# Kernel tuning notes

Hardware: AMD Instinct MI355X
Metric: run time of the kernel (lower is better)

Reference implementation:

```python
import jax, jax.numpy as jnp
import numpy as np

B, D = 4096, 1024
TEMPERATURE = 0.07


def setup_inputs() -> dict:
    key = jax.random.key(0)
    k1, k2, k3, k4, k5, k6 = jax.random.split(key, 6)
    return {
        "mri_features": jax.random.normal(k1, (B, D), dtype=jnp.float32),
        "pet_features": jax.random.normal(k2, (B, D), dtype=jnp.float32),
        "labels": jax.random.randint(k3, (B,), 0, 3, dtype=jnp.int64),
        "subtype_mri": jax.random.randint(k4, (B,), 0, 4, dtype=jnp.int64),
        "subtype_pet": jax.random.randint(k5, (B,), 0, 4, dtype=jnp.int64),
        "clinical_similarity": jax.random.uniform(k6, (B, B), dtype=jnp.float32),
    }


def _build_weights(labels, subtype_mri, subtype_pet, clinical_similarity):
    # vectorized form of the O(B^2) python loop
    same_label = labels[:, None] == labels[None, :]
    label_zero = labels[:, None] == 0
    sub_match = (subtype_mri[:, None] == subtype_mri[None, :]) & (
        subtype_pet[:, None] == subtype_pet[None, :]
    )
    n = labels.shape[0]
    not_diag = ~jnp.eye(n, dtype=bool)
    mask = same_label & (label_zero | sub_match) & not_diag
    weights = jnp.where(mask, clinical_similarity, 0.0)
    row_sums = weights.sum(axis=1, keepdims=True)
    row_sums = jnp.where(row_sums == 0, 1.0, row_sums)
    return weights / row_sums


def _contrastive(fi, fj, weights):
    fi = fi / jnp.linalg.norm(fi, axis=1, keepdims=True)
    fj = fj / jnp.linalg.norm(fj, axis=1, keepdims=True)
    sim = jnp.matmul(fi, fj.T) / TEMPERATURE  # [B, B]
    log_sm = jax.nn.log_softmax(sim, axis=1)
    return -jnp.sum(weights * log_sm) / fi.shape[0]


def reference(mri_features, pet_features, labels, subtype_mri, subtype_pet, clinical_similarity):
    weights = _build_weights(labels, subtype_mri, subtype_pet, clinical_similarity)
    pairs = [
        (mri_features, pet_features),
        (pet_features, mri_features),
        (mri_features, mri_features),
        (pet_features, pet_features),
    ]
    total = 0.0
    for fi, fj in pairs:
        total = total + _contrastive(fi, fj, weights)
    return total / len(pairs)
```

## Files before the change

### kernel.cpp

```cpp
#include <hip/hip_runtime.h>
#include <hip/hip_bf16.h>
#include <math.h>

typedef __attribute__((ext_vector_type(8))) short bf16x8;
typedef __attribute__((ext_vector_type(4))) short bf16x4;
typedef __attribute__((ext_vector_type(4))) float f32x4;

#define NB 4096
#define ND 1024
#define INV_T 14.2857142857142857f

__device__ inline unsigned short f2bf(float x) {
    __hip_bfloat16 h = __float2bfloat16(x);
    return *reinterpret_cast<unsigned short*>(&h);
}
__device__ inline float bf2f(unsigned short u) {
    unsigned v = ((unsigned)u) << 16;
    return __uint_as_float(v);
}
__device__ inline void gload16(const void* g, void* l) {
    __builtin_amdgcn_global_load_lds(
        (const __attribute__((address_space(1))) void*)g,
        (__attribute__((address_space(3))) void*)l, 16, 0, 0);
}

__global__ __launch_bounds__(256) void norm_kernel(
        const float* __restrict__ M, const float* __restrict__ P,
        unsigned char* __restrict__ Mf, unsigned char* __restrict__ Pf) {
    int row = blockIdx.x & (NB - 1);
    const float* src = (blockIdx.x < NB) ? M : P;
    unsigned char* dst = (blockIdx.x < NB) ? Mf : Pf;
    int tid = threadIdx.x;
    float4 v = ((const float4*)(src + (size_t)row * ND))[tid];
    float ss = v.x * v.x + v.y * v.y + v.z * v.z + v.w * v.w;
    for (int off = 32; off; off >>= 1) ss += __shfl_down(ss, off);
    __shared__ float red[4];
    int lane = tid & 63, w = tid >> 6;
    if (lane == 0) red[w] = ss;
    __syncthreads();
    float rn = rsqrtf(red[0] + red[1] + red[2] + red[3]);
    int p = __builtin_amdgcn_cvt_pk_fp8_f32(v.x * rn, v.y * rn, 0, false);
    p = __builtin_amdgcn_cvt_pk_fp8_f32(v.z * rn, v.w * rn, p, true);
    ((int*)dst)[row * 256 + tid] = p;
}

__global__ __launch_bounds__(256) void key_kernel(
        const int* __restrict__ labels, const int* __restrict__ sm,
        const int* __restrict__ sp, int* __restrict__ code) {
    int i = blockIdx.x * 256 + threadIdx.x;
    if (i < NB) {
        int l = labels[i];
        code[i] = (l == 0) ? 0x40000000 : (1 + l + (sm[i] << 8) + (sp[i] << 16));
    }
}

__global__ __launch_bounds__(256) void rowsumw_kernel(
        const float* __restrict__ cs, const int* __restrict__ code,
        unsigned short* __restrict__ W, float* __restrict__ flag) {
    int i = blockIdx.x;
    int ci = code[i];
    int tid = threadIdx.x;
    const float4* row = (const float4*)(cs + (size_t)i * NB);
    const int4* c4 = (const int4*)code;
    float4 v[4];
    int4 cj[4];
    float s = 0.f;
#pragma unroll
    for (int k = 0; k < 4; ++k) {
        int t = tid + k * 256;
        v[k] = row[t];
        cj[k] = c4[t];
        int j = t * 4;
        if (cj[k].x == ci && j + 0 != i) s += v[k].x;
        if (cj[k].y == ci && j + 1 != i) s += v[k].y;
        if (cj[k].z == ci && j + 2 != i) s += v[k].z;
        if (cj[k].w == ci && j + 3 != i) s += v[k].w;
    }
    for (int off = 1; off < 64; off <<= 1) s += __shfl_xor(s, off);
    __shared__ float red[4];
    int lane = tid & 63, w = tid >> 6;
    if (lane == 0) red[w] = s;
    __syncthreads();
    float tot = red[0] + red[1] + red[2] + red[3];
    float inv = (tot > 0.f) ? 1.f / tot : 0.f;
#pragma unroll
    for (int k = 0; k < 4; ++k) {
        int t = tid + k * 256;
        int j = t * 4;
        ushort4 o;
        o.x = (cj[k].x == ci && j + 0 != i) ? f2bf(v[k].x * inv) : (unsigned short)0;
        o.y = (cj[k].y == ci && j + 1 != i) ? f2bf(v[k].y * inv) : (unsigned short)0;
        o.z = (cj[k].z == ci && j + 2 != i) ? f2bf(v[k].z * inv) : (unsigned short)0;
        o.w = (cj[k].w == ci && j + 3 != i) ? f2bf(v[k].w * inv) : (unsigned short)0;
        *(ushort4*)&W[(size_t)i * NB + j] = o;
    }
    if (tid == 0) flag[i] = (tot > 0.f) ? 1.f : 0.f;
}

__global__ __launch_bounds__(256) void symw_kernel(unsigned short* __restrict__ W) {
    __shared__ unsigned short Ta[64][72], Tb[64][72];
    int b = blockIdx.x;
    int ti = 0, t = b;
    while (t >= 64 - ti) { t -= 64 - ti; ++ti; }
    int tj = ti + t;
    size_t ra = (size_t)ti * 64, rb = (size_t)tj * 64;
    int tid = threadIdx.x;
    int r = tid >> 2, c0 = (tid & 3) * 16;
    int4 a0 = *(const int4*)&W[(ra + r) * NB + rb + c0];
    int4 a1 = *(const int4*)&W[(ra + r) * NB + rb + c0 + 8];
    int4 b0 = *(const int4*)&W[(rb + r) * NB + ra + c0];
    int4 b1 = *(const int4*)&W[(rb + r) * NB + ra + c0 + 8];
    *(int4*)&Ta[r][c0] = a0;  *(int4*)&Ta[r][c0 + 8] = a1;
    *(int4*)&Tb[r][c0] = b0;  *(int4*)&Tb[r][c0 + 8] = b1;
    __syncthreads();
    unsigned short oa[16], ob[16];
#pragma unroll
    for (int c = 0; c < 16; ++c) {
        int cc = c0 + c;
        oa[c] = f2bf(bf2f(Ta[r][cc]) + bf2f(Tb[cc][r]));
        ob[c] = f2bf(bf2f(Tb[r][cc]) + bf2f(Ta[cc][r]));
    }
    *(int4*)&W[(ra + r) * NB + rb + c0]     = *(int4*)&oa[0];
    *(int4*)&W[(ra + r) * NB + rb + c0 + 8] = *(int4*)&oa[8];
    *(int4*)&W[(rb + r) * NB + ra + c0]     = *(int4*)&ob[0];
    *(int4*)&W[(rb + r) * NB + ra + c0 + 8] = *(int4*)&ob[8];
}

__global__ __launch_bounds__(512) void mega_gemm(
        const unsigned char* __restrict__ Mf, const unsigned char* __restrict__ Pf,
        const unsigned short* __restrict__ Wg,
        float* __restrict__ rowsum1, float* __restrict__ colsum1,
        float* __restrict__ rowsum3, float* __restrict__ rowsum4,
        float* __restrict__ dots) {
    __shared__ char smem[98304] __attribute__((aligned(16)));

    int tid = threadIdx.x;
    int lane = tid & 63, w = tid >> 6;
    int wm = w >> 1, wn = w & 1;
    int lr = lane & 15, lg = lane >> 4;

    int b = (blockIdx.x & 7) * 132 + (blockIdx.x >> 3);
    int bi, bj, ch, mode;
    const unsigned char *A, *Bm;
    if (b < 512) {
        bi = b >> 5;
        bj = (b & 31) >> 1;
        ch = b & 1;
        A = Mf; Bm = Pf; mode = 0;
    } else {
        int s = b - 512;
        int md = (s >= 272) ? 1 : 0;
        s -= md * 272;
        ch = s & 1;
        int t = s >> 1;
        bi = 0;
        while (t >= 16 - bi) { t -= 16 - bi; ++bi; }
        bj = bi + t;
        A = md ? Pf : Mf; Bm = A;
        mode = 1 + md;
    }
    bool offdiag = (bi != bj);
    size_t rowBase = (size_t)bi * 256;
    size_t colBase = (size_t)bj * 256 + ch * 128;
    float* rowTgt = (mode == 0) ? rowsum1 : ((mode == 1) ? rowsum3 : rowsum4);
    float* colTgt = (mode == 0) ? colsum1 : rowTgt;

    int sr = lane >> 2;
    int scs = (lane & 3) ^ (sr & 3) ^ ((sr >> 2) & 3);
    const unsigned char* gA = A + (rowBase + w * 32 + sr) * ND + scs * 16;
    const unsigned char* gB = Bm + (colBase + w * 16 + sr) * ND + scs * 16;

    f32x4 acc[4][4] = {};

#define STAGE(bufi, t) {                                                    \
        int k0_ = (t) * 64;                                                 \
        char* baseA_ = smem + (bufi) * 24576;                               \
        char* baseB_ = baseA_ + 16384;                                      \
        gload16(gA + k0_,                  baseA_ + (w * 2    ) * 1024);    \
        gload16(gA + (size_t)16 * ND + k0_, baseA_ + (w * 2 + 1) * 1024);   \
        gload16(gB + k0_,                  baseB_ + w * 1024);              \
    }
#define COMPUTE(bufi) {                                                     \
        const unsigned char* sA = (const unsigned char*)(smem + (bufi) * 24576); \
        const unsigned char* sB = sA + 16384;                               \
        int rx = (lr & 3) ^ ((lr >> 2) & 3);                                \
        _Pragma("unroll")                                                   \
        for (int ks = 0; ks < 2; ++ks) {                                    \
            int cp = (((ks * 2) + (lg >> 1)) ^ rx) * 16 + (lg & 1) * 8;     \
            long av[4], bv[4];                                              \
            _Pragma("unroll")                                               \
            for (int n = 0; n < 4; ++n)                                     \
                bv[n] = *(const long*)&sB[(wn * 64 + n * 16 + lr) * 64 + cp]; \
            _Pragma("unroll")                                               \
            for (int i = 0; i < 4; ++i)                                     \
                av[i] = *(const long*)&sA[(wm * 64 + i * 16 + lr) * 64 + cp]; \
            _Pragma("unroll")                                               \
            for (int i = 0; i < 4; ++i)                                     \
                _Pragma("unroll")                                           \
                for (int n = 0; n < 4; ++n)                                 \
                    acc[i][n] = __builtin_amdgcn_mfma_f32_16x16x32_fp8_fp8( \
                        av[i], bv[n], acc[i][n], 0, 0, 0);                  \
        }                                                                   \
    }
#define BAR __builtin_amdgcn_s_barrier()

    STAGE(0, 0); STAGE(1, 1); STAGE(2, 2);
    asm volatile("s_waitcnt vmcnt(6)" ::: "memory"); BAR;
    for (int t = 0; t < 13; ++t) {
        STAGE((t + 3) & 3, t + 3);
        COMPUTE(t & 3);
        asm volatile("s_waitcnt vmcnt(6)" ::: "memory"); BAR;
    }
    COMPUTE(13 & 3);
    asm volatile("s_waitcnt vmcnt(3)" ::: "memory"); BAR;
    COMPUTE(14 & 3);
    asm volatile("s_waitcnt vmcnt(0)" ::: "memory"); BAR;
    COMPUTE(15 & 3);
    __syncthreads();
#undef STAGE
#undef COMPUTE
#undef BAR

    unsigned short* wl = (unsigned short*)smem;
    float d1 = 0.f;
    float cexp[4] = {0.f, 0.f, 0.f, 0.f};

#pragma unroll
    for (int c = 0; c < 8; ++c) {
        int q = w * 8 + c;
        int sw = 4 * q + (lane >> 4);
        int gchunk = (lane & 15) ^ (sw & 7);
        gload16(Wg + (rowBase + sw) * (size_t)NB + colBase + gchunk * 8,
                smem + q * 1024);
    }
    __syncthreads();
#pragma unroll
    for (int m = 0; m < 4; ++m) {
        float rexp[4] = {0.f, 0.f, 0.f, 0.f};
#pragma unroll
        for (int n = 0; n < 4; ++n) {
            int jl = wn * 64 + n * 16 + lr;
#pragma unroll
            for (int r = 0; r < 4; ++r) {
                int rl = wm * 64 + m * 16 + lg * 4 + r;
                float sim = acc[m][n][r] * INV_T;
                float e = __expf(sim - INV_T);
                rexp[r] += e;
                cexp[n] += e;
                int ck = (jl >> 3) ^ (rl & 7);
                d1 += bf2f(wl[rl * 128 + ck * 8 + (jl & 7)]) * sim;
            }
        }
#pragma unroll
        for (int r = 0; r < 4; ++r) {
            float v = rexp[r];
            v += __shfl_xor(v, 1); v += __shfl_xor(v, 2);
            v += __shfl_xor(v, 4); v += __shfl_xor(v, 8);
            if (lr == 0)
                atomicAdd(&rowTgt[rowBase + wm * 64 + m * 16 + lg * 4 + r], v);
        }
    }

    if (mode == 0 || offdiag) {
#pragma unroll
        for (int n = 0; n < 4; ++n) {
            float v = cexp[n];
            v += __shfl_xor(v, 16); v += __shfl_xor(v, 32);
            if (lg == 0)
                atomicAdd(&colTgt[colBase + wn * 64 + n * 16 + lr], v);
        }
    }

    float dtot = (mode != 0 && !offdiag) ? 0.5f * d1 : d1;
    for (int off = 32; off; off >>= 1) dtot += __shfl_xor(dtot, off);
    if (lane == 0) {
        if (mode == 0) atomicAdd(&dots[0], dtot);
        else           atomicAdd(&dots[1 + mode], dtot);
    }
}

__global__ __launch_bounds__(256) void finalize_kernel(
        const float* __restrict__ rowsum1, const float* __restrict__ colsum1,
        const float* __restrict__ rowsum3, const float* __restrict__ rowsum4,
        const float* __restrict__ flag, const float* __restrict__ dots,
        float* __restrict__ out) {
    int tid = threadIdx.x;
    float l = 0.f;
    for (int i = tid; i < NB; i += 256) {
        if (flag[i] != 0.f) {
            l += 4.f * INV_T + logf(rowsum1[i]) + logf(colsum1[i]) +
                 logf(rowsum3[i]) + logf(rowsum4[i]);
        }
    }
    for (int off = 32; off; off >>= 1) l += __shfl_down(l, off);
    __shared__ float red[4];
    int lane = tid & 63, w = tid >> 6;
    if (lane == 0) red[w] = l;
    __syncthreads();
    if (tid == 0) {
        float L = red[0] + red[1] + red[2] + red[3];
        float dt = dots[0] + dots[1] + dots[2] + dots[3];
        out[0] = (L - dt) / (4.0f * (float)NB);
    }
}

extern "C" void kernel_launch(void* const* d_in, const int* in_sizes, int n_in,
                              void* d_out, int out_size, void* d_ws, size_t ws_size,
                              hipStream_t stream) {
    const float* M = (const float*)d_in[0];
    const float* P = (const float*)d_in[1];
    const int* labels = (const int*)d_in[2];
    const int* sm = (const int*)d_in[3];
    const int* sp = (const int*)d_in[4];
    const float* cs = (const float*)d_in[5];
    float* out = (float*)d_out;

    char* ws = (char*)d_ws;
    unsigned char* Mf = (unsigned char*)ws;
    unsigned char* Pf = (unsigned char*)(ws + (size_t)4 * 1024 * 1024);
    unsigned short* W = (unsigned short*)(ws + (size_t)16 * 1024 * 1024);
    char* p = ws + (size_t)48 * 1024 * 1024;
    int* code = (int*)p;        p += 16384;
    float* flag = (float*)p;    p += 16384;
    float* rowsum1 = (float*)p; p += 16384;
    float* colsum1 = (float*)p; p += 16384;
    float* rowsum3 = (float*)p; p += 16384;
    float* rowsum4 = (float*)p; p += 16384;
    float* dots = (float*)p;

    hipMemsetAsync(rowsum1, 0, 4 * 16384 + 256, stream);

    norm_kernel<<<2 * NB, 256, 0, stream>>>(M, P, Mf, Pf);
    key_kernel<<<NB / 256, 256, 0, stream>>>(labels, sm, sp, code);
    rowsumw_kernel<<<NB, 256, 0, stream>>>(cs, code, W, flag);
    symw_kernel<<<2080, 256, 0, stream>>>(W);

    mega_gemm<<<1056, 512, 0, stream>>>(Mf, Pf, W, rowsum1, colsum1,
                                        rowsum3, rowsum4, dots);

    finalize_kernel<<<1, 256, 0, stream>>>(rowsum1, colsum1, rowsum3, rowsum4,
                                           flag, dots, out);
}
```

Measured before the change: 217.3 us.

## Shrink GEMM tiles to 128x128 with 256-thread blocks and 3-stage pipeline

Each fused GEMM block now computes a 128x128 tile with 4 waves instead of a 256x128 tile with 8 waves. The shared-memory ring drops from four 24KB stages to three 16KB stages, and launch bounds ask for 3 blocks per CU. The symmetric MM/PP passes enumerate 128-granularity upper-triangle tiles, which cuts redundant work on diagonal tiles and gives 2080 blocks for better CU balance. The trade-off is less operand reuse per loaded byte and a shallower prefetch pipeline.

```diff
diff --git a/kernel.cpp b/kernel.cpp
--- a/kernel.cpp
+++ b/kernel.cpp
@@ -126,63 +126,61 @@
     *(int4*)&W[(rb + r) * NB + ra + c0 + 8] = *(int4*)&ob[8];
 }
 
-__global__ __launch_bounds__(512) void mega_gemm(
+__global__ __launch_bounds__(256, 3) void mega_gemm(
         const unsigned char* __restrict__ Mf, const unsigned char* __restrict__ Pf,
         const unsigned short* __restrict__ Wg,
         float* __restrict__ rowsum1, float* __restrict__ colsum1,
         float* __restrict__ rowsum3, float* __restrict__ rowsum4,
         float* __restrict__ dots) {
-    __shared__ char smem[98304] __attribute__((aligned(16)));
+    __shared__ char smem[49152] __attribute__((aligned(16)));
 
     int tid = threadIdx.x;
     int lane = tid & 63, w = tid >> 6;
     int wm = w >> 1, wn = w & 1;
     int lr = lane & 15, lg = lane >> 4;
 
-    int b = (blockIdx.x & 7) * 132 + (blockIdx.x >> 3);
-    int bi, bj, ch, mode;
+    int b = (blockIdx.x & 7) * 260 + (blockIdx.x >> 3);
+    int bi, bj, mode;
     const unsigned char *A, *Bm;
-    if (b < 512) {
+    if (b < 1024) {
         bi = b >> 5;
-        bj = (b & 31) >> 1;
-        ch = b & 1;
+        bj = b & 31;
         A = Mf; Bm = Pf; mode = 0;
     } else {
-        int s = b - 512;
-        int md = (s >= 272) ? 1 : 0;
-        s -= md * 272;
-        ch = s & 1;
-        int t = s >> 1;
+        int s = b - 1024;
+        int md = (s >= 528) ? 1 : 0;
+        s -= md * 528;
         bi = 0;
-        while (t >= 16 - bi) { t -= 16 - bi; ++bi; }
-        bj = bi + t;
+        while (s >= 32 - bi) { s -= 32 - bi; ++bi; }
+        bj = bi + s;
         A = md ? Pf : Mf; Bm = A;
         mode = 1 + md;
     }
     bool offdiag = (bi != bj);
-    size_t rowBase = (size_t)bi * 256;
-    size_t colBase = (size_t)bj * 256 + ch * 128;
+    size_t rowBase = (size_t)bi * 128;
+    size_t colBase = (size_t)bj * 128;
     float* rowTgt = (mode == 0) ? rowsum1 : ((mode == 1) ? rowsum3 : rowsum4);
     float* colTgt = (mode == 0) ? colsum1 : rowTgt;
 
     int sr = lane >> 2;
     int scs = (lane & 3) ^ (sr & 3) ^ ((sr >> 2) & 3);
     const unsigned char* gA = A + (rowBase + w * 32 + sr) * ND + scs * 16;
-    const unsigned char* gB = Bm + (colBase + w * 16 + sr) * ND + scs * 16;
+    const unsigned char* gB = Bm + (colBase + w * 32 + sr) * ND + scs * 16;
 
     f32x4 acc[4][4] = {};
 
 #define STAGE(bufi, t) {                                                    \
         int k0_ = (t) * 64;                                                 \
-        char* baseA_ = smem + (bufi) * 24576;                               \
-        char* baseB_ = baseA_ + 16384;                                      \
-        gload16(gA + k0_,                  baseA_ + (w * 2    ) * 1024);    \
+        char* baseA_ = smem + (bufi) * 16384;                               \
+        char* baseB_ = baseA_ + 8192;                                       \
+        gload16(gA + k0_,                   baseA_ + (w * 2    ) * 1024);   \
         gload16(gA + (size_t)16 * ND + k0_, baseA_ + (w * 2 + 1) * 1024);   \
-        gload16(gB + k0_,                  baseB_ + w * 1024);              \
+        gload16(gB + k0_,                   baseB_ + (w * 2    ) * 1024);   \
+        gload16(gB + (size_t)16 * ND + k0_, baseB_ + (w * 2 + 1) * 1024);   \
     }
 #define COMPUTE(bufi) {                                                     \
-        const unsigned char* sA = (const unsigned char*)(smem + (bufi) * 24576); \
-        const unsigned char* sB = sA + 16384;                               \
+        const unsigned char* sA = (const unsigned char*)(smem + (bufi) * 16384); \
+        const unsigned char* sB = sA + 8192;                                \
         int rx = (lr & 3) ^ ((lr >> 2) & 3);                                \
         _Pragma("unroll")                                                   \
         for (int ks = 0; ks < 2; ++ks) {                                    \
@@ -204,18 +202,16 @@
     }
 #define BAR __builtin_amdgcn_s_barrier()
 
-    STAGE(0, 0); STAGE(1, 1); STAGE(2, 2);
-    asm volatile("s_waitcnt vmcnt(6)" ::: "memory"); BAR;
-    for (int t = 0; t < 13; ++t) {
-        STAGE((t + 3) & 3, t + 3);
-        COMPUTE(t & 3);
-        asm volatile("s_waitcnt vmcnt(6)" ::: "memory"); BAR;
-    }
-    COMPUTE(13 & 3);
-    asm volatile("s_waitcnt vmcnt(3)" ::: "memory"); BAR;
-    COMPUTE(14 & 3);
+    STAGE(0, 0); STAGE(1, 1);
+    asm volatile("s_waitcnt vmcnt(4)" ::: "memory"); BAR;
+    for (int t = 0; t < 14; ++t) {
+        STAGE((t + 2) % 3, t + 2);
+        COMPUTE(t % 3);
+        asm volatile("s_waitcnt vmcnt(4)" ::: "memory"); BAR;
+    }
+    COMPUTE(14 % 3);
     asm volatile("s_waitcnt vmcnt(0)" ::: "memory"); BAR;
-    COMPUTE(15 & 3);
+    COMPUTE(15 % 3);
     __syncthreads();
 #undef STAGE
 #undef COMPUTE
@@ -335,7 +331,7 @@
     rowsumw_kernel<<<NB, 256, 0, stream>>>(cs, code, W, flag);
     symw_kernel<<<2080, 256, 0, stream>>>(W);
 
-    mega_gemm<<<1056, 512, 0, stream>>>(Mf, Pf, W, rowsum1, colsum1,
+    mega_gemm<<<2080, 256, 0, stream>>>(Mf, Pf, W, rowsum1, colsum1,
                                         rowsum3, rowsum4, dots);
 
     finalize_kernel<<<1, 256, 0, stream>>>(rowsum1, colsum1, rowsum3, rowsum4,
```

After: 208.3 us. -4.2%, faster.
